# Performance work log

Hardware: AMD Instinct MI355X
Metric: run time of the kernel (lower is better)

## Reference

```python
import jax, jax.numpy as jnp
import numpy as np
from jax.ops import segment_sum

NUM_GRAPHS = 64


def _leaky_relu(x):
    return jnp.where(x >= 0, x, 0.01 * x)


def setup_inputs() -> dict:
    key = jax.random.key(0)
    ks = jax.random.split(key, 8)
    N, E, D = 100000, 1600000, 128
    x = jax.random.normal(ks[0], (N, D), dtype=jnp.float32)
    edge_index = jax.random.randint(ks[1], (2, E), 0, N, dtype=jnp.int64)
    batch = jnp.sort(jax.random.randint(ks[2], (N,), 0, NUM_GRAPHS, dtype=jnp.int64))
    s = 1.0 / np.sqrt(D)
    W1 = jax.random.normal(ks[3], (D, D), dtype=jnp.float32) * s
    b1 = jnp.zeros((D,), dtype=jnp.float32)
    W2 = jax.random.normal(ks[4], (D, D), dtype=jnp.float32) * s
    b2 = jnp.zeros((D,), dtype=jnp.float32)
    fcW = jax.random.normal(ks[5], (D, 1), dtype=jnp.float32) * s
    fcb = jnp.zeros((1,), dtype=jnp.float32)
    return {"x": x, "edge_index": edge_index, "batch": batch,
            "W1": W1, "b1": b1, "W2": W2, "b2": b2, "fcW": fcW, "fcb": fcb}


def reference(x, edge_index, batch, W1, b1, W2, b2, fcW, fcb):
    N = x.shape[0]
    # GCNConv: add self-loops, symmetric normalization D^-1/2 A D^-1/2
    loop = jnp.arange(N, dtype=edge_index.dtype)
    row = jnp.concatenate([edge_index[0], loop])  # source j
    col = jnp.concatenate([edge_index[1], loop])  # target i
    deg = segment_sum(jnp.ones_like(col, dtype=x.dtype), col, num_segments=N)
    dis = jax.lax.rsqrt(deg)  # deg >= 1 due to self-loops
    norm = dis[row] * dis[col]  # [E+N]

    def conv(h, W, b):
        h = h @ W                               # [N, D'] linear transform
        msg = h[row] * norm[:, None]            # gather + scale
        agg = segment_sum(msg, col, num_segments=N)  # scatter-add
        return agg + b

    h = _leaky_relu(conv(x, W1, b1))
    h = _leaky_relu(conv(h, W2, b2))

    # global_mean_pool over batch ids
    sums = segment_sum(h, batch, num_segments=NUM_GRAPHS)
    cnts = segment_sum(jnp.ones((N,), dtype=h.dtype), batch, num_segments=NUM_GRAPHS)
    pooled = sums / jnp.maximum(cnts, 1.0)[:, None]
    return pooled @ fcW + fcb  # [NUM_GRAPHS, 1]
```

## Files before the change

### kernel.cpp

```cpp
#include <hip/hip_runtime.h>
#include <hip/hip_bf16.h>
#include <math.h>

#define D 128
#define NUM_GRAPHS 64
#define CHUNK 8192
#define BUCK_SH 8
#define BUCK_N 256
#define BCAP 8192
#define PSLICE 8
#define HROW 136

typedef __bf16 bf16x8 __attribute__((ext_vector_type(8)));
typedef __bf16 bf16x2 __attribute__((ext_vector_type(2)));
typedef float f32x4 __attribute__((ext_vector_type(4)));
typedef float f32x2 __attribute__((ext_vector_type(2)));

__device__ inline unsigned char f32_to_fp8(float x) {
    int pk = __builtin_amdgcn_cvt_pk_fp8_f32(x, x, 0, false);
    return (unsigned char)(pk & 0xff);
}
template <bool HI>
__device__ inline f32x2 fp8x2_to_f32(unsigned int us) {
    return __builtin_amdgcn_cvt_pk_f32_fp8(us, HI);
}
__device__ inline f32x2 fp8x2_to_f32_us(unsigned short us) {
    return __builtin_amdgcn_cvt_pk_f32_fp8((unsigned int)us, false);
}

__global__ void k_prepW(const float* __restrict__ Wa, const float* __restrict__ Wb,
                        __bf16* __restrict__ WfA, __bf16* __restrict__ WfB,
                        float* __restrict__ pooled,
                        int* __restrict__ gcur,
                        const int* __restrict__ batch, int* __restrict__ gstart, int N) {
    int gid = blockIdx.x * 256 + threadIdx.x;
    if (gid < NUM_GRAPHS * D) pooled[gid] = 0.f;
    if (gid < 512) gcur[gid] = 0;
    if (gid >= 16384 && gid <= 16384 + NUM_GRAPHS) {
        int g = gid - 16384;
        int lo = 0, hi = N;
        while (lo < hi) { int mid = (lo + hi) >> 1; if (batch[mid] < g) lo = mid + 1; else hi = mid; }
        gstart[g] = lo;
    }
    if (gid >= 32768) return;
    const float* W = (gid < 16384) ? Wa : Wb;
    __bf16* Wf = (gid < 16384) ? WfA : WfB;
    int idx = gid & 16383;
    int j = idx & 7, lane = (idx >> 3) & 63, kc = (idx >> 9) & 3, ft = idx >> 11;
    int k = kc * 32 + (lane >> 4) * 8 + j;
    int f = ft * 16 + (lane & 15);
    Wf[idx] = (__bf16)W[k * D + f];
}

template <typename T>
__device__ __forceinline__ void gemm_body(int bid, int tid, const T* __restrict__ X,
                                          const __bf16* __restrict__ Wfrag,
                                          unsigned char* __restrict__ Y8, int N) {
    int w = tid >> 6, lane = tid & 63;
    int quad = lane >> 4, m = lane & 15;
    int nodeA = bid * 64 + w * 16 + m;
    if (nodeA >= N) nodeA = N - 1;

    bf16x8 a[4];
#pragma unroll
    for (int kc = 0; kc < 4; kc++) {
        int kb = kc * 32 + quad * 8;
        if constexpr (sizeof(T) == 4) {
            f32x4 x0 = *(const f32x4*)(X + (size_t)nodeA * D + kb);
            f32x4 x1 = *(const f32x4*)(X + (size_t)nodeA * D + kb + 4);
#pragma unroll
            for (int j = 0; j < 4; j++) { a[kc][j] = (__bf16)x0[j]; a[kc][4 + j] = (__bf16)x1[j]; }
        } else {
            a[kc] = *(const bf16x8*)(X + (size_t)nodeA * D + kb);
        }
    }

    f32x4 d[8];
#pragma unroll
    for (int ft = 0; ft < 8; ft++) {
        d[ft] = (f32x4){0.f, 0.f, 0.f, 0.f};
#pragma unroll
        for (int kc = 0; kc < 4; kc++) {
            bf16x8 b = *(const bf16x8*)(Wfrag + (((ft << 2) | kc) * 64 + lane) * 8);
            d[ft] = __builtin_amdgcn_mfma_f32_16x16x32_bf16(a[kc], b, d[ft], 0, 0, 0);
        }
    }

#pragma unroll
    for (int r = 0; r < 4; r++) {
        int node = bid * 64 + w * 16 + quad * 4 + r;
        if (node < N) {
#pragma unroll
            for (int ft = 0; ft < 8; ft++)
                Y8[(size_t)node * D + ft * 16 + m] = f32_to_fp8(d[ft][r]);
        }
    }
}

__launch_bounds__(256)
__global__ void k_bin_gemm(const int* __restrict__ ei, int* __restrict__ gcur,
                           int* __restrict__ bbuf, int nbuck, int E, int nchunk,
                           const float* __restrict__ X, const __bf16* __restrict__ Wfrag,
                           unsigned char* __restrict__ Y8, int N) {
    __shared__ int h[512];
    __shared__ int base[512];

    if (blockIdx.x >= nchunk) {
        gemm_body<float>(blockIdx.x - nchunk, threadIdx.x, X, Wfrag, Y8, N);
        return;
    }

    int tid = threadIdx.x;
    for (int b = tid; b < nbuck; b += 256) h[b] = 0;
    __syncthreads();
    int lo = blockIdx.x * CHUNK;
    if (lo + CHUNK <= E) {
        const int4* c4 = (const int4*)(ei + E + lo);
#pragma unroll 2
        for (int i = tid; i < CHUNK / 4; i += 256) {
            int4 c = c4[i];
            atomicAdd(&h[c.x >> BUCK_SH], 1);
            atomicAdd(&h[c.y >> BUCK_SH], 1);
            atomicAdd(&h[c.z >> BUCK_SH], 1);
            atomicAdd(&h[c.w >> BUCK_SH], 1);
        }
    } else {
        for (int i = tid; i < CHUNK; i += 256) {
            int e = lo + i;
            if (e < E) atomicAdd(&h[ei[E + e] >> BUCK_SH], 1);
        }
    }
    __syncthreads();
    for (int b = tid; b < nbuck; b += 256) {
        base[b] = atomicAdd(&gcur[b], h[b]);
        h[b] = 0;
    }
    __syncthreads();
    if (lo + CHUNK <= E) {
        const int4* r4 = (const int4*)(ei + lo);
        const int4* c4 = (const int4*)(ei + E + lo);
#pragma unroll 2
        for (int i = tid; i < CHUNK / 4; i += 256) {
            int4 r = r4[i];
            int4 c = c4[i];
            int rr[4] = {r.x, r.y, r.z, r.w};
            int cc[4] = {c.x, c.y, c.z, c.w};
#pragma unroll
            for (int u = 0; u < 4; u++) {
                int b = cc[u] >> BUCK_SH;
                int pos = base[b] + atomicAdd(&h[b], 1);
                if (pos < BCAP) bbuf[(size_t)b * BCAP + pos] = rr[u] | ((cc[u] & (BUCK_N - 1)) << 17);
            }
        }
    } else {
        for (int i = tid; i < CHUNK; i += 256) {
            int e = lo + i;
            if (e < E) {
                int r = ei[e], c = ei[E + e];
                int b = c >> BUCK_SH;
                int pos = base[b] + atomicAdd(&h[b], 1);
                if (pos < BCAP) bbuf[(size_t)b * BCAP + pos] = r | ((c & (BUCK_N - 1)) << 17);
            }
        }
    }
}

__global__ void k_place(const int* __restrict__ bbuf, const int* __restrict__ gcur,
                        int* __restrict__ esrc,
                        int* __restrict__ cnt, int* __restrict__ offs,
                        float* __restrict__ dis, unsigned char* __restrict__ z1, int N) {
    __shared__ int h[256];
    __shared__ int sc[256];
    __shared__ int cur[256];
    __shared__ float sdis[256];
    int b = blockIdx.x, tid = threadIdx.x;
    int start = b * BCAP;
    int count = gcur[b]; if (count > BCAP) count = BCAP;
    int end = start + count;
    h[tid] = 0;
    __syncthreads();
    for (int i = start + tid; i < end; i += 256) atomicAdd(&h[(bbuf[i] >> 17) & 255], 1);
    __syncthreads();
    int local = h[tid];
    sc[tid] = local;
    __syncthreads();
    for (int off = 1; off < 256; off <<= 1) {
        int xv = (tid >= off) ? sc[tid - off] : 0;
        __syncthreads();
        sc[tid] += xv;
        __syncthreads();
    }
    int excl = sc[tid] - local;
    cur[tid] = start + excl;
    int c = b * 256 + tid;
    float dv = rsqrtf(1.0f + (float)local);
    sdis[tid] = dv;
    if (c < N) {
        cnt[c]  = local;
        offs[c] = start + excl;
        dis[c]  = dv;
    }
    __syncthreads();
    for (int i = start + tid; i < end; i += 256) {
        int p = bbuf[i];
        int pos = atomicAdd(&cur[(p >> 17) & 255], 1);
        esrc[pos] = p & 0x1FFFF;
    }
    int nrows = N - b * 256; if (nrows > 256) nrows = 256; if (nrows < 0) nrows = 0;
    unsigned int* zp = (unsigned int*)(z1 + (size_t)b * 256 * D);
    for (int i = tid; i < nrows * 32; i += 256) {
        int row = i >> 5;
        float s = sdis[row];
        unsigned int v = zp[i];
        f32x2 lo = fp8x2_to_f32<false>(v);
        f32x2 hi = fp8x2_to_f32<true>(v);
        unsigned int u = (unsigned int)__builtin_amdgcn_cvt_pk_fp8_f32(lo[0] * s, lo[1] * s, 0, false);
        u = (unsigned int)__builtin_amdgcn_cvt_pk_fp8_f32(hi[0] * s, hi[1] * s, (int)u, true);
        zp[i] = u;
    }
}

__launch_bounds__(256)
__global__ void k_agg_gemm(const unsigned char* __restrict__ Hs8,
                           const int* __restrict__ offs, const int* __restrict__ cnt,
                           const float* __restrict__ dis, const int* __restrict__ esrc,
                           const float* __restrict__ bias,
                           const __bf16* __restrict__ Wfrag,
                           unsigned char* __restrict__ Y8, int N) {
    __shared__ __bf16 hl[32 * HROW];
    int tid = threadIdx.x;
    int w = tid >> 6, lane = tid & 63;
    int node0 = blockIdx.x * 32 + w * 8;
    float b0 = bias[lane * 2], b1v = bias[lane * 2 + 1];

    for (int nn = 0; nn < 8; nn++) {
        int node = node0 + nn;
        if (node < N) {
            int start = offs[node];
            int len = cnt[node];
            float di = dis[node];
            f32x2 h = fp8x2_to_f32_us(*(const unsigned short*)(Hs8 + (size_t)node * D + lane * 2));
            float acc0 = h[0];
            float acc1 = h[1];

            for (int k0 = 0; k0 < len; k0 += 64) {
                int mm = len - k0; if (mm > 64) mm = 64;
                int ep = esrc[start + k0 + (lane < mm ? lane : 0)];
                int j = 0;
                for (; j + 16 <= mm; j += 16) {
                    int s[16]; unsigned short hv[16];
#pragma unroll
                    for (int u = 0; u < 16; u++) s[u] = __shfl(ep, j + u);
#pragma unroll
                    for (int u = 0; u < 16; u++) hv[u] = *(const unsigned short*)(Hs8 + (size_t)s[u] * D + lane * 2);
#pragma unroll
                    for (int u = 0; u < 16; u++) { f32x2 f = fp8x2_to_f32_us(hv[u]); acc0 += f[0]; acc1 += f[1]; }
                }
                for (; j + 4 <= mm; j += 4) {
                    int s[4]; unsigned short hv[4];
#pragma unroll
                    for (int u = 0; u < 4; u++) s[u] = __shfl(ep, j + u);
#pragma unroll
                    for (int u = 0; u < 4; u++) hv[u] = *(const unsigned short*)(Hs8 + (size_t)s[u] * D + lane * 2);
#pragma unroll
                    for (int u = 0; u < 4; u++) { f32x2 f = fp8x2_to_f32_us(hv[u]); acc0 += f[0]; acc1 += f[1]; }
                }
                for (; j < mm; j++) {
                    int s = __shfl(ep, j);
                    f32x2 f = fp8x2_to_f32_us(*(const unsigned short*)(Hs8 + (size_t)s * D + lane * 2));
                    acc0 += f[0]; acc1 += f[1];
                }
            }

            acc0 = acc0 * di + b0;
            acc1 = acc1 * di + b1v;
            acc0 = acc0 >= 0.f ? acc0 : 0.01f * acc0;
            acc1 = acc1 >= 0.f ? acc1 : 0.01f * acc1;
            bf16x2 o; o[0] = (__bf16)acc0; o[1] = (__bf16)acc1;
            *(bf16x2*)&hl[(w * 8 + nn) * HROW + lane * 2] = o;
        } else {
            bf16x2 z; z[0] = (__bf16)0.f; z[1] = (__bf16)0.f;
            *(bf16x2*)&hl[(w * 8 + nn) * HROW + lane * 2] = z;
        }
    }
    __syncthreads();

    int quad = lane >> 4, m = lane & 15;
    int rtile = w & 1, fthalf = w >> 1;
    int lrow = rtile * 16 + m;
    bf16x8 a[4];
#pragma unroll
    for (int kc = 0; kc < 4; kc++)
        a[kc] = *(const bf16x8*)&hl[lrow * HROW + kc * 32 + quad * 8];

    int nb = blockIdx.x * 32 + rtile * 16 + quad * 4;
    float scv[4];
#pragma unroll
    for (int r = 0; r < 4; r++) scv[r] = (nb + r < N) ? dis[nb + r] : 0.f;

#pragma unroll
    for (int ft = 0; ft < 4; ft++) {
        int gft = fthalf * 4 + ft;
        f32x4 dacc = (f32x4){0.f, 0.f, 0.f, 0.f};
#pragma unroll
        for (int kc = 0; kc < 4; kc++) {
            bf16x8 b = *(const bf16x8*)(Wfrag + (((gft << 2) | kc) * 64 + lane) * 8);
            dacc = __builtin_amdgcn_mfma_f32_16x16x32_bf16(a[kc], b, dacc, 0, 0, 0);
        }
#pragma unroll
        for (int r = 0; r < 4; r++) {
            int node = nb + r;
            if (node < N)
                Y8[(size_t)node * D + gft * 16 + m] = f32_to_fp8(dacc[r] * scv[r]);
        }
    }
}

__launch_bounds__(256)
__global__ void k_agg(const unsigned char* __restrict__ Hs8, __bf16* __restrict__ O,
                      const int* __restrict__ offs, const int* __restrict__ cnt,
                      const float* __restrict__ dis, const int* __restrict__ esrc,
                      const float* __restrict__ bias, int N) {
    int wave = (blockIdx.x * 256 + threadIdx.x) >> 6;
    int lane = threadIdx.x & 63;
    int node0 = wave * 8;
    float b0 = bias[lane * 2], b1 = bias[lane * 2 + 1];

    for (int nn = 0; nn < 8; nn++) {
        int node = node0 + nn;
        if (node >= N) return;
        int start = offs[node];
        int len = cnt[node];
        float di = dis[node];
        f32x2 h = fp8x2_to_f32_us(*(const unsigned short*)(Hs8 + (size_t)node * D + lane * 2));
        float acc0 = h[0];
        float acc1 = h[1];

        for (int k0 = 0; k0 < len; k0 += 64) {
            int mm = len - k0; if (mm > 64) mm = 64;
            int ep = esrc[start + k0 + (lane < mm ? lane : 0)];
            int j = 0;
            for (; j + 16 <= mm; j += 16) {
                int s[16]; unsigned short hv[16];
#pragma unroll
                for (int u = 0; u < 16; u++) s[u] = __shfl(ep, j + u);
#pragma unroll
                for (int u = 0; u < 16; u++) hv[u] = *(const unsigned short*)(Hs8 + (size_t)s[u] * D + lane * 2);
#pragma unroll
                for (int u = 0; u < 16; u++) { f32x2 f = fp8x2_to_f32_us(hv[u]); acc0 += f[0]; acc1 += f[1]; }
            }
            for (; j + 4 <= mm; j += 4) {
                int s[4]; unsigned short hv[4];
#pragma unroll
                for (int u = 0; u < 4; u++) s[u] = __shfl(ep, j + u);
#pragma unroll
                for (int u = 0; u < 4; u++) hv[u] = *(const unsigned short*)(Hs8 + (size_t)s[u] * D + lane * 2);
#pragma unroll
                for (int u = 0; u < 4; u++) { f32x2 f = fp8x2_to_f32_us(hv[u]); acc0 += f[0]; acc1 += f[1]; }
            }
            for (; j < mm; j++) {
                int s = __shfl(ep, j);
                f32x2 f = fp8x2_to_f32_us(*(const unsigned short*)(Hs8 + (size_t)s * D + lane * 2));
                acc0 += f[0]; acc1 += f[1];
            }
        }

        acc0 = acc0 * di + b0;
        acc1 = acc1 * di + b1;
        acc0 = acc0 >= 0.f ? acc0 : 0.01f * acc0;
        acc1 = acc1 >= 0.f ? acc1 : 0.01f * acc1;
        bf16x2 o; o[0] = (__bf16)acc0; o[1] = (__bf16)acc1;
        *(bf16x2*)(O + (size_t)node * D + lane * 2) = o;
    }
}

__launch_bounds__(256)
__global__ void k_pool(const __bf16* __restrict__ H, const int* __restrict__ gstart,
                       float* __restrict__ pooled) {
    __shared__ float sdata[256 * 9];
    int g = blockIdx.x / PSLICE;
    int slice = blockIdx.x - g * PSLICE;
    int gs = gstart[g], ge = gstart[g + 1];
    int cg = ge - gs;
    int r0 = gs + (int)((long long)cg * slice / PSLICE);
    int r1 = gs + (int)((long long)cg * (slice + 1) / PSLICE);
    int t = threadIdx.x;
    int rg = t >> 4, fb = t & 15;

    float acc[8];
#pragma unroll
    for (int j = 0; j < 8; j++) acc[j] = 0.f;
    for (int r = r0 + rg; r < r1; r += 16) {
        bf16x8 v = *(const bf16x8*)(H + (size_t)r * D + fb * 8);
#pragma unroll
        for (int j = 0; j < 8; j++) acc[j] += (float)v[j];
    }
#pragma unroll
    for (int j = 0; j < 8; j++) sdata[t * 9 + j] = acc[j];
    __syncthreads();
#pragma unroll
    for (int s = 128; s >= 16; s >>= 1) {
        if (t < s) {
#pragma unroll
            for (int j = 0; j < 8; j++) sdata[t * 9 + j] += sdata[(t + s) * 9 + j];
        }
        __syncthreads();
    }
    if (t < 16) {
#pragma unroll
        for (int j = 0; j < 8; j++) atomicAdd(&pooled[g * D + t * 8 + j], sdata[t * 9 + j]);
    }
}

__launch_bounds__(64)
__global__ void k_fc(const float* __restrict__ pooled, const int* __restrict__ gstart,
                     const float* __restrict__ fcW, const float* __restrict__ fcb,
                     float* __restrict__ out) {
    int t = threadIdx.x;
    float s = 0.f;
#pragma unroll 8
    for (int k = 0; k < D; k += 4) {
        f32x4 pv = *(const f32x4*)(pooled + t * D + k);
        f32x4 wv = *(const f32x4*)(fcW + k);
        s += pv[0] * wv[0] + pv[1] * wv[1] + pv[2] * wv[2] + pv[3] * wv[3];
    }
    float c = (float)(gstart[t + 1] - gstart[t]);
    out[t] = s / fmaxf(c, 1.0f) + fcb[0];
}

extern "C" void kernel_launch(void* const* d_in, const int* in_sizes, int n_in,
                              void* d_out, int out_size, void* d_ws, size_t ws_size,
                              hipStream_t stream) {
    const float* x    = (const float*)d_in[0];
    const int*   ei   = (const int*)d_in[1];
    const int*   batch= (const int*)d_in[2];
    const float* W1   = (const float*)d_in[3];
    const float* b1   = (const float*)d_in[4];
    const float* W2   = (const float*)d_in[5];
    const float* b2   = (const float*)d_in[6];
    const float* fcW  = (const float*)d_in[7];
    const float* fcb  = (const float*)d_in[8];
    float* out = (float*)d_out;

    int N = in_sizes[0] / D;
    int E = in_sizes[1] / 2;

    int NBUCK  = (N + BUCK_N - 1) >> BUCK_SH;
    int NCHUNK = (E + CHUNK - 1) / CHUNK;

    char* p = (char*)d_ws;
    auto alloc = [&](size_t bytes) { char* r = p; p += (bytes + 255) & ~(size_t)255; return r; };
    int*    cnt    = (int*)   alloc((size_t)N * 4);
    int*    offs   = (int*)   alloc((size_t)N * 4);
    float*  dis    = (float*) alloc((size_t)N * 4);
    int*    gcur   = (int*)   alloc(512 * 4);
    int*    bbuf   = (int*)   alloc((size_t)NBUCK * BCAP * 4);
    int*    esrc   = (int*)   alloc((size_t)NBUCK * BCAP * 4);
    unsigned char* bufA8 = (unsigned char*)alloc((size_t)(NBUCK * BUCK_N) * D);
    unsigned char* bufC8 = (unsigned char*)alloc((size_t)N * D);
    __bf16* bufB   = (__bf16*)alloc((size_t)N * D * 2);
    __bf16* Wf1    = (__bf16*)alloc((size_t)D * D * 2);
    __bf16* Wf2    = (__bf16*)alloc((size_t)D * D * 2);
    float*  pooled = (float*) alloc((size_t)NUM_GRAPHS * D * 4);
    int*    gstart = (int*)   alloc((NUM_GRAPHS + 1) * 4);

    int gblocks = (N + 63) / 64;
    int ablocks = (N + 31) / 32;

    k_prepW<<<129, 256, 0, stream>>>(W1, W2, Wf1, Wf2, pooled, gcur, batch, gstart, N);

    k_bin_gemm<<<NCHUNK + gblocks, 256, 0, stream>>>(ei, gcur, bbuf, NBUCK, E, NCHUNK,
                                                     x, Wf1, bufA8, N);
    k_place<<<NBUCK, 256, 0, stream>>>(bbuf, gcur, esrc, cnt, offs, dis, bufA8, N);

    k_agg_gemm<<<ablocks, 256, 0, stream>>>(bufA8, offs, cnt, dis, esrc, b1, Wf2, bufC8, N);

    k_agg<<<ablocks, 256, 0, stream>>>(bufC8, bufB, offs, cnt, dis, esrc, b2, N);

    k_pool<<<NUM_GRAPHS * PSLICE, 256, 0, stream>>>(bufB, gstart, pooled);
    k_fc<<<1, 64, 0, stream>>>(pooled, gstart, fcW, fcb, out);
}
```

Measured before the change: 281.7 us.

## Fuse mean-pool into layer-2 aggregation and fold weight prep into other kernels

The second aggregation now accumulates leaky-relu outputs straight into per-graph pooled sums, using sorted batch ids, shared-memory partials and atomics. This removes the bf16 intermediate write and the separate pool kernel. W1 is converted to bf16 fragments in LDS by each GEMM block, W2 conversion moves into k_place, and k_prepW is replaced by memsets, with the gstart binary search moved into k_fc. This cuts two launches and one N×D round trip, at the cost of redundant W1 conversion per GEMM block, extra LDS use that may lower occupancy of the binning kernel, and global atomics.

```diff
diff --git a/kernel.cpp b/kernel.cpp
--- a/kernel.cpp
+++ b/kernel.cpp
@@ -8,7 +8,6 @@
 #define BUCK_SH 8
 #define BUCK_N 256
 #define BCAP 8192
-#define PSLICE 8
 #define HROW 136
 
 typedef __bf16 bf16x8 __attribute__((ext_vector_type(8)));
@@ -28,89 +27,75 @@
     return __builtin_amdgcn_cvt_pk_f32_fp8((unsigned int)us, false);
 }
 
-__global__ void k_prepW(const float* __restrict__ Wa, const float* __restrict__ Wb,
-                        __bf16* __restrict__ WfA, __bf16* __restrict__ WfB,
-                        float* __restrict__ pooled,
-                        int* __restrict__ gcur,
-                        const int* __restrict__ batch, int* __restrict__ gstart, int N) {
-    int gid = blockIdx.x * 256 + threadIdx.x;
-    if (gid < NUM_GRAPHS * D) pooled[gid] = 0.f;
-    if (gid < 512) gcur[gid] = 0;
-    if (gid >= 16384 && gid <= 16384 + NUM_GRAPHS) {
-        int g = gid - 16384;
-        int lo = 0, hi = N;
-        while (lo < hi) { int mid = (lo + hi) >> 1; if (batch[mid] < g) lo = mid + 1; else hi = mid; }
-        gstart[g] = lo;
-    }
-    if (gid >= 32768) return;
-    const float* W = (gid < 16384) ? Wa : Wb;
-    __bf16* Wf = (gid < 16384) ? WfA : WfB;
-    int idx = gid & 16383;
-    int j = idx & 7, lane = (idx >> 3) & 63, kc = (idx >> 9) & 3, ft = idx >> 11;
-    int k = kc * 32 + (lane >> 4) * 8 + j;
-    int f = ft * 16 + (lane & 15);
-    Wf[idx] = (__bf16)W[k * D + f];
-}
-
-template <typename T>
-__device__ __forceinline__ void gemm_body(int bid, int tid, const T* __restrict__ X,
-                                          const __bf16* __restrict__ Wfrag,
-                                          unsigned char* __restrict__ Y8, int N) {
-    int w = tid >> 6, lane = tid & 63;
-    int quad = lane >> 4, m = lane & 15;
-    int nodeA = bid * 64 + w * 16 + m;
-    if (nodeA >= N) nodeA = N - 1;
-
-    bf16x8 a[4];
-#pragma unroll
-    for (int kc = 0; kc < 4; kc++) {
-        int kb = kc * 32 + quad * 8;
-        if constexpr (sizeof(T) == 4) {
-            f32x4 x0 = *(const f32x4*)(X + (size_t)nodeA * D + kb);
-            f32x4 x1 = *(const f32x4*)(X + (size_t)nodeA * D + kb + 4);
-#pragma unroll
-            for (int j = 0; j < 4; j++) { a[kc][j] = (__bf16)x0[j]; a[kc][4 + j] = (__bf16)x1[j]; }
-        } else {
-            a[kc] = *(const bf16x8*)(X + (size_t)nodeA * D + kb);
-        }
-    }
-
-    f32x4 d[8];
-#pragma unroll
-    for (int ft = 0; ft < 8; ft++) {
-        d[ft] = (f32x4){0.f, 0.f, 0.f, 0.f};
-#pragma unroll
-        for (int kc = 0; kc < 4; kc++) {
-            bf16x8 b = *(const bf16x8*)(Wfrag + (((ft << 2) | kc) * 64 + lane) * 8);
-            d[ft] = __builtin_amdgcn_mfma_f32_16x16x32_bf16(a[kc], b, d[ft], 0, 0, 0);
-        }
-    }
-
-#pragma unroll
-    for (int r = 0; r < 4; r++) {
-        int node = bid * 64 + w * 16 + quad * 4 + r;
-        if (node < N) {
-#pragma unroll
-            for (int ft = 0; ft < 8; ft++)
-                Y8[(size_t)node * D + ft * 16 + m] = f32_to_fp8(d[ft][r]);
-        }
-    }
+__device__ inline int wfrag_idx(int k, int f) {
+    int kc = k >> 5, quad = (k >> 3) & 3, j = k & 7;
+    int ft = f >> 4, m = f & 15;
+    int lane = quad * 16 + m;
+    return (((ft << 2) | kc) * 64 + lane) * 8 + j;
 }
 
 __launch_bounds__(256)
 __global__ void k_bin_gemm(const int* __restrict__ ei, int* __restrict__ gcur,
                            int* __restrict__ bbuf, int nbuck, int E, int nchunk,
-                           const float* __restrict__ X, const __bf16* __restrict__ Wfrag,
+                           const float* __restrict__ X, const float* __restrict__ W1,
                            unsigned char* __restrict__ Y8, int N) {
     __shared__ int h[512];
     __shared__ int base[512];
+    __shared__ __bf16 Wlds[16384];
+    int tid = threadIdx.x;
 
     if (blockIdx.x >= nchunk) {
-        gemm_body<float>(blockIdx.x - nchunk, threadIdx.x, X, Wfrag, Y8, N);
+        const float4* w4 = (const float4*)W1;
+        for (int i = tid; i < 4096; i += 256) {
+            float4 v = w4[i];
+            int bkf = i * 4;
+            int k = bkf >> 7, f0 = bkf & 127;
+            Wlds[wfrag_idx(k, f0 + 0)] = (__bf16)v.x;
+            Wlds[wfrag_idx(k, f0 + 1)] = (__bf16)v.y;
+            Wlds[wfrag_idx(k, f0 + 2)] = (__bf16)v.z;
+            Wlds[wfrag_idx(k, f0 + 3)] = (__bf16)v.w;
+        }
+        __syncthreads();
+
+        int bid = blockIdx.x - nchunk;
+        int w = tid >> 6, lane = tid & 63;
+        int quad = lane >> 4, m = lane & 15;
+        int nodeA = bid * 64 + w * 16 + m;
+        if (nodeA >= N) nodeA = N - 1;
+
+        bf16x8 a[4];
+#pragma unroll
+        for (int kc = 0; kc < 4; kc++) {
+            int kb = kc * 32 + quad * 8;
+            f32x4 x0 = *(const f32x4*)(X + (size_t)nodeA * D + kb);
+            f32x4 x1 = *(const f32x4*)(X + (size_t)nodeA * D + kb + 4);
+#pragma unroll
+            for (int j = 0; j < 4; j++) { a[kc][j] = (__bf16)x0[j]; a[kc][4 + j] = (__bf16)x1[j]; }
+        }
+
+        f32x4 d[8];
+#pragma unroll
+        for (int ft = 0; ft < 8; ft++) {
+            d[ft] = (f32x4){0.f, 0.f, 0.f, 0.f};
+#pragma unroll
+            for (int kc = 0; kc < 4; kc++) {
+                bf16x8 b = *(const bf16x8*)(Wlds + (((ft << 2) | kc) * 64 + lane) * 8);
+                d[ft] = __builtin_amdgcn_mfma_f32_16x16x32_bf16(a[kc], b, d[ft], 0, 0, 0);
+            }
+        }
+
+#pragma unroll
+        for (int r = 0; r < 4; r++) {
+            int node = bid * 64 + w * 16 + quad * 4 + r;
+            if (node < N) {
+#pragma unroll
+                for (int ft = 0; ft < 8; ft++)
+                    Y8[(size_t)node * D + ft * 16 + m] = f32_to_fp8(d[ft][r]);
+            }
+        }
         return;
     }
 
-    int tid = threadIdx.x;
     for (int b = tid; b < nbuck; b += 256) h[b] = 0;
     __syncthreads();
     int lo = blockIdx.x * CHUNK;
@@ -168,12 +153,24 @@
 __global__ void k_place(const int* __restrict__ bbuf, const int* __restrict__ gcur,
                         int* __restrict__ esrc,
                         int* __restrict__ cnt, int* __restrict__ offs,
-                        float* __restrict__ dis, unsigned char* __restrict__ z1, int N) {
+                        float* __restrict__ dis, unsigned char* __restrict__ z1,
+                        const float* __restrict__ W2, __bf16* __restrict__ Wf2, int N) {
     __shared__ int h[256];
     __shared__ int sc[256];
     __shared__ int cur[256];
     __shared__ float sdis[256];
     int b = blockIdx.x, tid = threadIdx.x;
+
+    for (int q = tid; q < 42; q += 256) {
+        int idx = b * 42 + q;
+        if (idx < 16384) {
+            int j = idx & 7, lane = (idx >> 3) & 63, kc = (idx >> 9) & 3, ft = idx >> 11;
+            int k = kc * 32 + (lane >> 4) * 8 + j;
+            int f = ft * 16 + (lane & 15);
+            Wf2[idx] = (__bf16)W2[k * D + f];
+        }
+    }
+
     int start = b * BCAP;
     int count = gcur[b]; if (count > BCAP) count = BCAP;
     int end = start + count;
@@ -317,115 +314,117 @@
 }
 
 __launch_bounds__(256)
-__global__ void k_agg(const unsigned char* __restrict__ Hs8, __bf16* __restrict__ O,
-                      const int* __restrict__ offs, const int* __restrict__ cnt,
-                      const float* __restrict__ dis, const int* __restrict__ esrc,
-                      const float* __restrict__ bias, int N) {
-    int wave = (blockIdx.x * 256 + threadIdx.x) >> 6;
-    int lane = threadIdx.x & 63;
-    int node0 = wave * 8;
+__global__ void k_agg_pool(const unsigned char* __restrict__ Hs8,
+                           const int* __restrict__ offs, const int* __restrict__ cnt,
+                           const float* __restrict__ dis, const int* __restrict__ esrc,
+                           const float* __restrict__ bias,
+                           const int* __restrict__ batch, float* __restrict__ pooled, int N) {
+    __shared__ float accL[2][128];
+    int tid = threadIdx.x;
+    int w = tid >> 6, lane = tid & 63;
+    int node0b = blockIdx.x * 32;
+    int node0 = node0b + w * 8;
     float b0 = bias[lane * 2], b1 = bias[lane * 2 + 1];
+    int gbase = node0b < N ? node0b : N - 1;
+    int g_lo = batch[gbase];
+    accL[tid >> 7][tid & 127] = 0.f;
+    __syncthreads();
+
+    float sA0 = 0.f, sA1 = 0.f, sB0 = 0.f, sB1 = 0.f;
 
     for (int nn = 0; nn < 8; nn++) {
         int node = node0 + nn;
-        if (node >= N) return;
-        int start = offs[node];
-        int len = cnt[node];
-        float di = dis[node];
-        f32x2 h = fp8x2_to_f32_us(*(const unsigned short*)(Hs8 + (size_t)node * D + lane * 2));
-        float acc0 = h[0];
-        float acc1 = h[1];
-
-        for (int k0 = 0; k0 < len; k0 += 64) {
-            int mm = len - k0; if (mm > 64) mm = 64;
-            int ep = esrc[start + k0 + (lane < mm ? lane : 0)];
-            int j = 0;
-            for (; j + 16 <= mm; j += 16) {
-                int s[16]; unsigned short hv[16];
-#pragma unroll
-                for (int u = 0; u < 16; u++) s[u] = __shfl(ep, j + u);
-#pragma unroll
-                for (int u = 0; u < 16; u++) hv[u] = *(const unsigned short*)(Hs8 + (size_t)s[u] * D + lane * 2);
-#pragma unroll
-                for (int u = 0; u < 16; u++) { f32x2 f = fp8x2_to_f32_us(hv[u]); acc0 += f[0]; acc1 += f[1]; }
-            }
-            for (; j + 4 <= mm; j += 4) {
-                int s[4]; unsigned short hv[4];
-#pragma unroll
-                for (int u = 0; u < 4; u++) s[u] = __shfl(ep, j + u);
-#pragma unroll
-                for (int u = 0; u < 4; u++) hv[u] = *(const unsigned short*)(Hs8 + (size_t)s[u] * D + lane * 2);
-#pragma unroll
-                for (int u = 0; u < 4; u++) { f32x2 f = fp8x2_to_f32_us(hv[u]); acc0 += f[0]; acc1 += f[1]; }
-            }
-            for (; j < mm; j++) {
-                int s = __shfl(ep, j);
-                f32x2 f = fp8x2_to_f32_us(*(const unsigned short*)(Hs8 + (size_t)s * D + lane * 2));
-                acc0 += f[0]; acc1 += f[1];
-            }
-        }
-
-        acc0 = acc0 * di + b0;
-        acc1 = acc1 * di + b1;
-        acc0 = acc0 >= 0.f ? acc0 : 0.01f * acc0;
-        acc1 = acc1 >= 0.f ? acc1 : 0.01f * acc1;
-        bf16x2 o; o[0] = (__bf16)acc0; o[1] = (__bf16)acc1;
-        *(bf16x2*)(O + (size_t)node * D + lane * 2) = o;
-    }
-}
-
-__launch_bounds__(256)
-__global__ void k_pool(const __bf16* __restrict__ H, const int* __restrict__ gstart,
-                       float* __restrict__ pooled) {
-    __shared__ float sdata[256 * 9];
-    int g = blockIdx.x / PSLICE;
-    int slice = blockIdx.x - g * PSLICE;
-    int gs = gstart[g], ge = gstart[g + 1];
-    int cg = ge - gs;
-    int r0 = gs + (int)((long long)cg * slice / PSLICE);
-    int r1 = gs + (int)((long long)cg * (slice + 1) / PSLICE);
-    int t = threadIdx.x;
-    int rg = t >> 4, fb = t & 15;
-
-    float acc[8];
-#pragma unroll
-    for (int j = 0; j < 8; j++) acc[j] = 0.f;
-    for (int r = r0 + rg; r < r1; r += 16) {
-        bf16x8 v = *(const bf16x8*)(H + (size_t)r * D + fb * 8);
-#pragma unroll
-        for (int j = 0; j < 8; j++) acc[j] += (float)v[j];
-    }
-#pragma unroll
-    for (int j = 0; j < 8; j++) sdata[t * 9 + j] = acc[j];
-    __syncthreads();
-#pragma unroll
-    for (int s = 128; s >= 16; s >>= 1) {
-        if (t < s) {
-#pragma unroll
-            for (int j = 0; j < 8; j++) sdata[t * 9 + j] += sdata[(t + s) * 9 + j];
-        }
-        __syncthreads();
-    }
-    if (t < 16) {
-#pragma unroll
-        for (int j = 0; j < 8; j++) atomicAdd(&pooled[g * D + t * 8 + j], sdata[t * 9 + j]);
-    }
-}
-
-__launch_bounds__(64)
-__global__ void k_fc(const float* __restrict__ pooled, const int* __restrict__ gstart,
+        if (node < N) {
+            int start = offs[node];
+            int len = cnt[node];
+            float di = dis[node];
+            f32x2 h = fp8x2_to_f32_us(*(const unsigned short*)(Hs8 + (size_t)node * D + lane * 2));
+            float acc0 = h[0];
+            float acc1 = h[1];
+
+            for (int k0 = 0; k0 < len; k0 += 64) {
+                int mm = len - k0; if (mm > 64) mm = 64;
+                int ep = esrc[start + k0 + (lane < mm ? lane : 0)];
+                int j = 0;
+                for (; j + 16 <= mm; j += 16) {
+                    int s[16]; unsigned short hv[16];
+#pragma unroll
+                    for (int u = 0; u < 16; u++) s[u] = __shfl(ep, j + u);
+#pragma unroll
+                    for (int u = 0; u < 16; u++) hv[u] = *(const unsigned short*)(Hs8 + (size_t)s[u] * D + lane * 2);
+#pragma unroll
+                    for (int u = 0; u < 16; u++) { f32x2 f = fp8x2_to_f32_us(hv[u]); acc0 += f[0]; acc1 += f[1]; }
+                }
+                for (; j + 4 <= mm; j += 4) {
+                    int s[4]; unsigned short hv[4];
+#pragma unroll
+                    for (int u = 0; u < 4; u++) s[u] = __shfl(ep, j + u);
+#pragma unroll
+                    for (int u = 0; u < 4; u++) hv[u] = *(const unsigned short*)(Hs8 + (size_t)s[u] * D + lane * 2);
+#pragma unroll
+                    for (int u = 0; u < 4; u++) { f32x2 f = fp8x2_to_f32_us(hv[u]); acc0 += f[0]; acc1 += f[1]; }
+                }
+                for (; j < mm; j++) {
+                    int s = __shfl(ep, j);
+                    f32x2 f = fp8x2_to_f32_us(*(const unsigned short*)(Hs8 + (size_t)s * D + lane * 2));
+                    acc0 += f[0]; acc1 += f[1];
+                }
+            }
+
+            acc0 = acc0 * di + b0;
+            acc1 = acc1 * di + b1;
+            acc0 = acc0 >= 0.f ? acc0 : 0.01f * acc0;
+            acc1 = acc1 >= 0.f ? acc1 : 0.01f * acc1;
+
+            int sel = batch[node] - g_lo;
+            if (sel == 0)      { sA0 += acc0; sA1 += acc1; }
+            else if (sel == 1) { sB0 += acc0; sB1 += acc1; }
+            else {
+                atomicAdd(&pooled[(g_lo + sel) * D + lane * 2],     acc0);
+                atomicAdd(&pooled[(g_lo + sel) * D + lane * 2 + 1], acc1);
+            }
+        }
+    }
+
+    atomicAdd(&accL[0][lane * 2],     sA0);
+    atomicAdd(&accL[0][lane * 2 + 1], sA1);
+    atomicAdd(&accL[1][lane * 2],     sB0);
+    atomicAdd(&accL[1][lane * 2 + 1], sB1);
+    __syncthreads();
+
+    if (tid < 128) {
+        atomicAdd(&pooled[g_lo * D + tid], accL[0][tid]);
+    } else {
+        float v = accL[1][tid - 128];
+        if (v != 0.f && g_lo + 1 < NUM_GRAPHS)
+            atomicAdd(&pooled[(g_lo + 1) * D + (tid - 128)], v);
+    }
+}
+
+__launch_bounds__(128)
+__global__ void k_fc(const float* __restrict__ pooled, const int* __restrict__ batch, int N,
                      const float* __restrict__ fcW, const float* __restrict__ fcb,
                      float* __restrict__ out) {
+    __shared__ int gs[NUM_GRAPHS + 1];
     int t = threadIdx.x;
-    float s = 0.f;
+    if (t <= NUM_GRAPHS) {
+        int g = t;
+        int lo = 0, hi = N;
+        while (lo < hi) { int mid = (lo + hi) >> 1; if (batch[mid] < g) lo = mid + 1; else hi = mid; }
+        gs[t] = lo;
+    }
+    __syncthreads();
+    if (t < NUM_GRAPHS) {
+        float s = 0.f;
 #pragma unroll 8
-    for (int k = 0; k < D; k += 4) {
-        f32x4 pv = *(const f32x4*)(pooled + t * D + k);
-        f32x4 wv = *(const f32x4*)(fcW + k);
-        s += pv[0] * wv[0] + pv[1] * wv[1] + pv[2] * wv[2] + pv[3] * wv[3];
-    }
-    float c = (float)(gstart[t + 1] - gstart[t]);
-    out[t] = s / fmaxf(c, 1.0f) + fcb[0];
+        for (int k = 0; k < D; k += 4) {
+            f32x4 pv = *(const f32x4*)(pooled + t * D + k);
+            f32x4 wv = *(const f32x4*)(fcW + k);
+            s += pv[0] * wv[0] + pv[1] * wv[1] + pv[2] * wv[2] + pv[3] * wv[3];
+        }
+        float c = (float)(gs[t + 1] - gs[t]);
+        out[t] = s / fmaxf(c, 1.0f) + fcb[0];
+    }
 }
 
 extern "C" void kernel_launch(void* const* d_in, const int* in_sizes, int n_in,
@@ -458,25 +457,23 @@
     int*    esrc   = (int*)   alloc((size_t)NBUCK * BCAP * 4);
     unsigned char* bufA8 = (unsigned char*)alloc((size_t)(NBUCK * BUCK_N) * D);
     unsigned char* bufC8 = (unsigned char*)alloc((size_t)N * D);
-    __bf16* bufB   = (__bf16*)alloc((size_t)N * D * 2);
-    __bf16* Wf1    = (__bf16*)alloc((size_t)D * D * 2);
     __bf16* Wf2    = (__bf16*)alloc((size_t)D * D * 2);
     float*  pooled = (float*) alloc((size_t)NUM_GRAPHS * D * 4);
-    int*    gstart = (int*)   alloc((NUM_GRAPHS + 1) * 4);
 
     int gblocks = (N + 63) / 64;
     int ablocks = (N + 31) / 32;
 
-    k_prepW<<<129, 256, 0, stream>>>(W1, W2, Wf1, Wf2, pooled, gcur, batch, gstart, N);
+    hipMemsetAsync(gcur, 0, 512 * 4, stream);
+    hipMemsetAsync(pooled, 0, (size_t)NUM_GRAPHS * D * 4, stream);
 
     k_bin_gemm<<<NCHUNK + gblocks, 256, 0, stream>>>(ei, gcur, bbuf, NBUCK, E, NCHUNK,
-                                                     x, Wf1, bufA8, N);
-    k_place<<<NBUCK, 256, 0, stream>>>(bbuf, gcur, esrc, cnt, offs, dis, bufA8, N);
+                                                     x, W1, bufA8, N);
+    k_place<<<NBUCK, 256, 0, stream>>>(bbuf, gcur, esrc, cnt, offs, dis, bufA8, W2, Wf2, N);
 
     k_agg_gemm<<<ablocks, 256, 0, stream>>>(bufA8, offs, cnt, dis, esrc, b1, Wf2, bufC8, N);
 
-    k_agg<<<ablocks, 256, 0, stream>>>(bufC8, bufB, offs, cnt, dis, esrc, b2, N);
-
-    k_pool<<<NUM_GRAPHS * PSLICE, 256, 0, stream>>>(bufB, gstart, pooled);
-    k_fc<<<1, 64, 0, stream>>>(pooled, gstart, fcW, fcb, out);
-}
+    k_agg_pool<<<ablocks, 256, 0, stream>>>(bufC8, offs, cnt, dis, esrc, b2,
+                                            batch, pooled, N);
+
+    k_fc<<<1, 128, 0, stream>>>(pooled, batch, N, fcW, fcb, out);
+}
```

After: 307.6 us. 9.2% more time.
